# Performance work log

Measured on AMD Instinct MI355X. Metric: run time of the kernel, lower is better.

The kernel has to match this reference:

```python
import jax, jax.numpy as jnp
import numpy as np

MUL_VAL = 4.0

def _fake_quant(v, qmin, qmax):
    # per-tensor float scale from abs-max (brevitas Int8*PerTensorFloat style)
    s = jnp.max(jnp.abs(v)) / 127.0
    q = jnp.clip(jnp.round(v / s), qmin, qmax) * s
    return q

def setup_inputs() -> dict:
    key = jax.random.key(0)
    k1, k2, k3 = jax.random.split(key, 3)
    N, IN, OUT = 8192, 4096, 4096
    x = jax.random.normal(k1, (N, IN), dtype=jnp.float32)
    W = jax.random.normal(k2, (OUT, IN), dtype=jnp.float32) * 0.02
    b = jax.random.normal(k3, (OUT,), dtype=jnp.float32) * 0.01
    return {"x": x, "W": W, "b": b}

def reference(x, W, b):
    # Int8ActPerTensorFloat: signed 8-bit, non-narrow range [-128, 127]
    qx = _fake_quant(x, -128.0, 127.0)
    # Int8WeightPerTensorFloat: signed 8-bit, narrow range [-127, 127]
    qw = _fake_quant(W, -127.0, 127.0)
    y = jnp.einsum('ni,oi->no', qx, qw) + b
    return MUL_VAL * y
```

## Files before the change

### kernel.cpp

```cpp
#include <hip/hip_runtime.h>

typedef int int4v __attribute__((ext_vector_type(4)));

#define BM 128
#define BN 128
#define BK 64

__device__ __forceinline__ void async_copy16(const void* g, void* l) {
  __builtin_amdgcn_global_load_lds((const __attribute__((address_space(1))) void*)g,
                                   (__attribute__((address_space(3))) void*)l, 16, 0, 0);
}

__global__ __launch_bounds__(256) void absmax2_kernel(
    const float* __restrict__ x, size_t n4x,
    const float* __restrict__ w, size_t n4w,
    unsigned* __restrict__ out, int xb) {
  const float4* src;
  size_t n4;
  unsigned* dst;
  int bid, nb;
  if ((int)blockIdx.x < xb) {
    src = (const float4*)x; n4 = n4x; dst = out; bid = blockIdx.x; nb = xb;
  } else {
    src = (const float4*)w; n4 = n4w; dst = out + 1; bid = blockIdx.x - xb; nb = gridDim.x - xb;
  }
  size_t i = (size_t)bid * blockDim.x + threadIdx.x;
  size_t stride = (size_t)nb * blockDim.x;
  float m = 0.0f;
  for (; i < n4; i += stride) {
    float4 v = src[i];
    m = fmaxf(m, fmaxf(fmaxf(fabsf(v.x), fabsf(v.y)), fmaxf(fabsf(v.z), fabsf(v.w))));
  }
#pragma unroll
  for (int off = 32; off > 0; off >>= 1)
    m = fmaxf(m, __shfl_down(m, off, 64));
  __shared__ float red[4];
  int wave = threadIdx.x >> 6, lane = threadIdx.x & 63;
  if (lane == 0) red[wave] = m;
  __syncthreads();
  if (threadIdx.x == 0) {
    m = fmaxf(fmaxf(red[0], red[1]), fmaxf(red[2], red[3]));
    atomicMax(dst, __float_as_uint(m));
  }
}

__global__ __launch_bounds__(256) void quant2_kernel(
    const float* __restrict__ x, char* __restrict__ qx, size_t nx,
    const float* __restrict__ w, char* __restrict__ qw, size_t nw,
    const unsigned* __restrict__ amax, int xb) {
  const float* src;
  char* dst;
  size_t n;
  float r, lo;
  int bid, nb;
  if ((int)blockIdx.x < xb) {
    src = x; dst = qx; n = nx; r = 127.0f / __uint_as_float(amax[0]);
    lo = -128.0f; bid = blockIdx.x; nb = xb;
  } else {
    src = w; dst = qw; n = nw; r = 127.0f / __uint_as_float(amax[1]);
    lo = -127.0f; bid = blockIdx.x - xb; nb = gridDim.x - xb;
  }
  size_t i = ((size_t)bid * blockDim.x + threadIdx.x) * 8;
  size_t stride = (size_t)nb * blockDim.x * 8;
  for (; i < n; i += stride) {
    float4 v0 = *(const float4*)(src + i);
    float4 v1 = *(const float4*)(src + i + 4);
    float f[8] = {v0.x, v0.y, v0.z, v0.w, v1.x, v1.y, v1.z, v1.w};
    unsigned w0 = 0, w1 = 0;
#pragma unroll
    for (int j = 0; j < 4; ++j) {
      int q0 = (int)fminf(fmaxf(rintf(f[j] * r), lo), 127.0f);
      int q1 = (int)fminf(fmaxf(rintf(f[4 + j] * r), lo), 127.0f);
      w0 |= (unsigned)(q0 & 0xff) << (8 * j);
      w1 |= (unsigned)(q1 & 0xff) << (8 * j);
    }
    uint2 u; u.x = w0; u.y = w1;
    *(uint2*)(dst + i) = u;
  }
}

__global__ __launch_bounds__(256) void gemm_i8_kernel(
    const char* __restrict__ qx, const char* __restrict__ qw,
    const float* __restrict__ bias, const unsigned* __restrict__ amax,
    float* __restrict__ out, int M, int N, int K) {
  __shared__ __align__(16) char As[BM * BK];
  __shared__ __align__(16) char Bs[BN * BK];
  int tid = threadIdx.x;
  int wave = tid >> 6, lane = tid & 63;
  int wm = (wave >> 1) * 64, wn = (wave & 1) * 64;

  int tilesM = M / BM, tilesN = N / BN;
  int T = tilesM * tilesN;
  int p = blockIdx.x;
  int tile;
  if ((T & 7) == 0) tile = (p & 7) * (T >> 3) + (p >> 3);
  else tile = p;
  int bm = (tile % tilesM) * BM;
  int bn = (tile / tilesM) * BN;

  int lrow = lane >> 2;
  int lcol = (lane & 3) * 16;
  const char* gA = qx + ((size_t)bm + lrow) * K + lcol;
  const char* gB = qw + ((size_t)bn + lrow) * K + lcol;
  int c0 = wave * 2;

  int4v acc[4][4] = {};

  int r = lane & 15;
  int kb = (lane >> 4) * 16;

  for (int kt = 0; kt < K; kt += BK) {
#pragma unroll
    for (int c = 0; c < 2; ++c) {
      int cc = c0 + c;
      async_copy16(gA + (size_t)(cc * 16) * K + kt, As + cc * 1024);
      async_copy16(gB + (size_t)(cc * 16) * K + kt, Bs + cc * 1024);
    }
    __syncthreads();
    int4v a[4], b[4];
#pragma unroll
    for (int i = 0; i < 4; ++i)
      a[i] = *(const int4v*)(As + (size_t)(wm + i * 16 + r) * BK + kb);
#pragma unroll
    for (int j = 0; j < 4; ++j)
      b[j] = *(const int4v*)(Bs + (size_t)(wn + j * 16 + r) * BK + kb);
#pragma unroll
    for (int i = 0; i < 4; ++i)
#pragma unroll
      for (int j = 0; j < 4; ++j)
        acc[i][j] = __builtin_amdgcn_mfma_i32_16x16x64_i8(a[i], b[j], acc[i][j], 0, 0, 0);
    __syncthreads();
  }

  float sx = __uint_as_float(amax[0]) / 127.0f;
  float sw = __uint_as_float(amax[1]) / 127.0f;
  float scale = 4.0f * sx * sw;
  int col = lane & 15;
  int rq = (lane >> 4) * 4;
#pragma unroll
  for (int j = 0; j < 4; ++j) {
    int gn = bn + wn + j * 16 + col;
    float b4 = 4.0f * bias[gn];
#pragma unroll
    for (int i = 0; i < 4; ++i) {
      size_t base = (size_t)(bm + wm + i * 16 + rq) * N + gn;
#pragma unroll
      for (int rr = 0; rr < 4; ++rr)
        __builtin_nontemporal_store(scale * (float)acc[i][j][rr] + b4,
                                    out + base + (size_t)rr * N);
    }
  }
}

extern "C" void kernel_launch(void* const* d_in, const int* in_sizes, int n_in,
                              void* d_out, int out_size, void* d_ws, size_t ws_size,
                              hipStream_t stream) {
  const float* x = (const float*)d_in[0];
  const float* W = (const float*)d_in[1];
  const float* b = (const float*)d_in[2];
  float* out = (float*)d_out;

  int Nv = in_sizes[2];
  int K = in_sizes[1] / Nv;
  int M = in_sizes[0] / K;

  size_t nx = (size_t)M * K, nw = (size_t)Nv * K;
  unsigned* amax = (unsigned*)d_ws;
  char* qx = (char*)d_ws + 256;
  char* qw = qx + nx;

  hipMemsetAsync(d_ws, 0, 8, stream);
  absmax2_kernel<<<1536, 256, 0, stream>>>(x, nx / 4, W, nw / 4, amax, 1024);
  quant2_kernel<<<3072, 256, 0, stream>>>(x, qx, nx, W, qw, nw, amax, 2048);
  gemm_i8_kernel<<<(M / BM) * (Nv / BN), 256, 0, stream>>>(qx, qw, b, amax, out, M, Nv, K);
}
```

Baseline: 488.0 us.

## Rewrite int8 GEMM with 256x256 tiles, double-buffered LDS and phased MFMA pipeline

The int8 GEMM moves from 128x128x64 single-buffered tiles to 256x256x128 tiles with 8 waves, double-buffered LDS, XOR-swizzled LDS layout, and an 8-phase schedule that interleaves async global-to-LDS staging with MFMA bursts under setprio and explicit vmcnt waits. The aim is to hide global load latency behind compute, raise arithmetic intensity per tile and avoid LDS bank conflicts. It uses 128 KB of LDS per block and many accumulator registers, which limits occupancy, and it needs K to be a multiple of 256 for the unrolled loop.

```diff
diff --git a/kernel.cpp b/kernel.cpp
--- a/kernel.cpp
+++ b/kernel.cpp
@@ -2,9 +2,9 @@
 
 typedef int int4v __attribute__((ext_vector_type(4)));
 
-#define BM 128
-#define BN 128
-#define BK 64
+#define BM 256
+#define BN 256
+#define BKB 128
 
 __device__ __forceinline__ void async_copy16(const void* g, void* l) {
   __builtin_amdgcn_global_load_lds((const __attribute__((address_space(1))) void*)g,
@@ -79,15 +79,80 @@
   }
 }
 
-__global__ __launch_bounds__(256) void gemm_i8_kernel(
+
+#define STAGE_A(buf_, t_, rowb_) do {                                          \
+    int r0_ = (rowb_) + wave * 8;                                              \
+    async_copy16(gA + (size_t)r0_ * K + (size_t)(t_) * BKB,                    \
+                 &As[buf_][r0_ * BKB]);                                        \
+    async_copy16(gA + (size_t)(r0_ + 64) * K + (size_t)(t_) * BKB,             \
+                 &As[buf_][(r0_ + 64) * BKB]);                                 \
+  } while (0)
+
+#define STAGE_B(buf_, t_, rowb_) do {                                          \
+    int r0_ = (rowb_) + wave * 8;                                              \
+    async_copy16(gB + (size_t)r0_ * K + (size_t)(t_) * BKB,                    \
+                 &Bs[buf_][r0_ * BKB]);                                        \
+    async_copy16(gB + (size_t)(r0_ + 64) * K + (size_t)(t_) * BKB,             \
+                 &Bs[buf_][(r0_ + 64) * BKB]);                                 \
+  } while (0)
+
+#define VM4 asm volatile("s_waitcnt vmcnt(4)" ::: "memory")
+#define VM0 asm volatile("s_waitcnt vmcnt(0)" ::: "memory")
+#define VMN ((void)0)
+#define NOSTG ((void)0)
+
+#define MFMA_I8 __builtin_amdgcn_mfma_i32_16x16x64_i8
+
+#define PHASE(bb_, mh_, nh_, STG, VMW) do {                                    \
+    asm volatile("" ::: "memory");                                             \
+    const char* Ab_ = &As[bb_][((mh_)*128 + wr * 64 + r16) * BKB];             \
+    const char* Bb_ = &Bs[bb_][((nh_)*128 + wc * 32 + r16) * BKB];             \
+    int4v a00_ = *(const int4v*)(Ab_ + 0 * 16 * BKB + slot0);                  \
+    int4v a01_ = *(const int4v*)(Ab_ + 0 * 16 * BKB + slot1);                  \
+    int4v a10_ = *(const int4v*)(Ab_ + 1 * 16 * BKB + slot0);                  \
+    int4v a11_ = *(const int4v*)(Ab_ + 1 * 16 * BKB + slot1);                  \
+    int4v a20_ = *(const int4v*)(Ab_ + 2 * 16 * BKB + slot0);                  \
+    int4v a21_ = *(const int4v*)(Ab_ + 2 * 16 * BKB + slot1);                  \
+    int4v a30_ = *(const int4v*)(Ab_ + 3 * 16 * BKB + slot0);                  \
+    int4v a31_ = *(const int4v*)(Ab_ + 3 * 16 * BKB + slot1);                  \
+    int4v b00_ = *(const int4v*)(Bb_ + 0 * 16 * BKB + slot0);                  \
+    int4v b01_ = *(const int4v*)(Bb_ + 0 * 16 * BKB + slot1);                  \
+    int4v b10_ = *(const int4v*)(Bb_ + 1 * 16 * BKB + slot0);                  \
+    int4v b11_ = *(const int4v*)(Bb_ + 1 * 16 * BKB + slot1);                  \
+    STG;                                                                       \
+    __builtin_amdgcn_s_barrier();                                              \
+    __builtin_amdgcn_s_setprio(1);                                             \
+    acc[mh_][nh_][0][0] = MFMA_I8(a00_, b00_, acc[mh_][nh_][0][0], 0, 0, 0);   \
+    acc[mh_][nh_][0][0] = MFMA_I8(a01_, b01_, acc[mh_][nh_][0][0], 0, 0, 0);   \
+    acc[mh_][nh_][0][1] = MFMA_I8(a00_, b10_, acc[mh_][nh_][0][1], 0, 0, 0);   \
+    acc[mh_][nh_][0][1] = MFMA_I8(a01_, b11_, acc[mh_][nh_][0][1], 0, 0, 0);   \
+    acc[mh_][nh_][1][0] = MFMA_I8(a10_, b00_, acc[mh_][nh_][1][0], 0, 0, 0);   \
+    acc[mh_][nh_][1][0] = MFMA_I8(a11_, b01_, acc[mh_][nh_][1][0], 0, 0, 0);   \
+    acc[mh_][nh_][1][1] = MFMA_I8(a10_, b10_, acc[mh_][nh_][1][1], 0, 0, 0);   \
+    acc[mh_][nh_][1][1] = MFMA_I8(a11_, b11_, acc[mh_][nh_][1][1], 0, 0, 0);   \
+    acc[mh_][nh_][2][0] = MFMA_I8(a20_, b00_, acc[mh_][nh_][2][0], 0, 0, 0);   \
+    acc[mh_][nh_][2][0] = MFMA_I8(a21_, b01_, acc[mh_][nh_][2][0], 0, 0, 0);   \
+    acc[mh_][nh_][2][1] = MFMA_I8(a20_, b10_, acc[mh_][nh_][2][1], 0, 0, 0);   \
+    acc[mh_][nh_][2][1] = MFMA_I8(a21_, b11_, acc[mh_][nh_][2][1], 0, 0, 0);   \
+    acc[mh_][nh_][3][0] = MFMA_I8(a30_, b00_, acc[mh_][nh_][3][0], 0, 0, 0);   \
+    acc[mh_][nh_][3][0] = MFMA_I8(a31_, b01_, acc[mh_][nh_][3][0], 0, 0, 0);   \
+    acc[mh_][nh_][3][1] = MFMA_I8(a30_, b10_, acc[mh_][nh_][3][1], 0, 0, 0);   \
+    acc[mh_][nh_][3][1] = MFMA_I8(a31_, b11_, acc[mh_][nh_][3][1], 0, 0, 0);   \
+    __builtin_amdgcn_s_setprio(0);                                             \
+    VMW;                                                                       \
+    asm volatile("" ::: "memory");                                             \
+    __builtin_amdgcn_s_barrier();                                              \
+  } while (0)
+
+__global__ __launch_bounds__(512, 2) void gemm_i8_kernel(
     const char* __restrict__ qx, const char* __restrict__ qw,
     const float* __restrict__ bias, const unsigned* __restrict__ amax,
     float* __restrict__ out, int M, int N, int K) {
-  __shared__ __align__(16) char As[BM * BK];
-  __shared__ __align__(16) char Bs[BN * BK];
-  int tid = threadIdx.x;
-  int wave = tid >> 6, lane = tid & 63;
-  int wm = (wave >> 1) * 64, wn = (wave & 1) * 64;
+  __shared__ __align__(16) char As[2][BM * BKB];
+  __shared__ __align__(16) char Bs[2][BN * BKB];
+  const int tid = threadIdx.x;
+  const int wave = tid >> 6, lane = tid & 63;
+  const int wr = wave >> 2, wc = wave & 3;
 
   int tilesM = M / BM, tilesN = N / BN;
   int T = tilesM * tilesN;
@@ -98,58 +163,71 @@
   int bm = (tile % tilesM) * BM;
   int bn = (tile / tilesM) * BN;
 
-  int lrow = lane >> 2;
-  int lcol = (lane & 3) * 16;
-  const char* gA = qx + ((size_t)bm + lrow) * K + lcol;
-  const char* gB = qw + ((size_t)bn + lrow) * K + lcol;
-  int c0 = wave * 2;
-
-  int4v acc[4][4] = {};
-
-  int r = lane & 15;
-  int kb = (lane >> 4) * 16;
-
-  for (int kt = 0; kt < K; kt += BK) {
-#pragma unroll
-    for (int c = 0; c < 2; ++c) {
-      int cc = c0 + c;
-      async_copy16(gA + (size_t)(cc * 16) * K + kt, As + cc * 1024);
-      async_copy16(gB + (size_t)(cc * 16) * K + kt, Bs + cc * 1024);
-    }
-    __syncthreads();
-    int4v a[4], b[4];
-#pragma unroll
-    for (int i = 0; i < 4; ++i)
-      a[i] = *(const int4v*)(As + (size_t)(wm + i * 16 + r) * BK + kb);
-#pragma unroll
-    for (int j = 0; j < 4; ++j)
-      b[j] = *(const int4v*)(Bs + (size_t)(wn + j * 16 + r) * BK + kb);
-#pragma unroll
-    for (int i = 0; i < 4; ++i)
-#pragma unroll
-      for (int j = 0; j < 4; ++j)
-        acc[i][j] = __builtin_amdgcn_mfma_i32_16x16x64_i8(a[i], b[j], acc[i][j], 0, 0, 0);
-    __syncthreads();
-  }
-
-  float sx = __uint_as_float(amax[0]) / 127.0f;
-  float sw = __uint_as_float(amax[1]) / 127.0f;
-  float scale = 4.0f * sx * sw;
-  int col = lane & 15;
-  int rq = (lane >> 4) * 4;
-#pragma unroll
-  for (int j = 0; j < 4; ++j) {
-    int gn = bn + wn + j * 16 + col;
-    float b4 = 4.0f * bias[gn];
-#pragma unroll
-    for (int i = 0; i < 4; ++i) {
-      size_t base = (size_t)(bm + wm + i * 16 + rq) * N + gn;
-#pragma unroll
-      for (int rr = 0; rr < 4; ++rr)
-        __builtin_nontemporal_store(scale * (float)acc[i][j][rr] + b4,
-                                    out + base + (size_t)rr * N);
-    }
-  }
+  const int grow = lane >> 3;
+  const int gcol = ((lane & 7) ^ grow) * 16;
+  const char* gA = qx + (size_t)(bm + grow) * K + gcol;
+  const char* gB = qw + (size_t)(bn + grow) * K + gcol;
+
+  const int r16 = lane & 15, hi = lane >> 4;
+  const int slot0 = ((0 + hi) ^ (lane & 7)) * 16;
+  const int slot1 = ((4 + hi) ^ (lane & 7)) * 16;
+
+  const int NT = K >> 7;
+
+  int4v acc[2][2][4][2] = {};
+
+  STAGE_A(0, 0, 0);
+  STAGE_B(0, 0, 0);
+  STAGE_A(0, 0, 128);
+  STAGE_B(0, 0, 128);
+  STAGE_A(1, 1, 0);
+  STAGE_B(1, 1, 0);
+  VM4;
+  __builtin_amdgcn_s_barrier();
+
+  int t = 0;
+  for (; t + 3 < NT; t += 2) {
+    PHASE(0, 0, 0, STAGE_A(1, t + 1, 128), VMN);
+    PHASE(0, 0, 1, STAGE_B(1, t + 1, 128), VMN);
+    PHASE(0, 1, 0, STAGE_A(0, t + 2, 0), VMN);
+    PHASE(0, 1, 1, STAGE_B(0, t + 2, 0), VM4);
+    PHASE(1, 0, 0, STAGE_A(0, t + 2, 128), VMN);
+    PHASE(1, 0, 1, STAGE_B(0, t + 2, 128), VMN);
+    PHASE(1, 1, 0, STAGE_A(1, t + 3, 0), VMN);
+    PHASE(1, 1, 1, STAGE_B(1, t + 3, 0), VM4);
+  }
+  PHASE(0, 0, 0, STAGE_A(1, NT - 1, 128), VMN);
+  PHASE(0, 0, 1, STAGE_B(1, NT - 1, 128), VMN);
+  PHASE(0, 1, 0, NOSTG, VMN);
+  PHASE(0, 1, 1, NOSTG, VM0);
+  PHASE(1, 0, 0, NOSTG, VMN);
+  PHASE(1, 0, 1, NOSTG, VMN);
+  PHASE(1, 1, 0, NOSTG, VMN);
+  PHASE(1, 1, 1, NOSTG, VMN);
+
+  float fx = __uint_as_float(amax[0]) * (1.0f / 127.0f);
+  float fw = __uint_as_float(amax[1]) * (1.0f / 127.0f);
+  float scale = 4.0f * fx * fw;
+  int col16 = lane & 15;
+  int rq = (lane >> 4) << 2;
+#pragma unroll
+  for (int mh = 0; mh < 2; ++mh)
+#pragma unroll
+    for (int nh = 0; nh < 2; ++nh)
+#pragma unroll
+      for (int n = 0; n < 2; ++n) {
+        int gn = bn + nh * 128 + wc * 32 + n * 16 + col16;
+        float b4 = 4.0f * bias[gn];
+#pragma unroll
+        for (int m = 0; m < 4; ++m) {
+          size_t base = (size_t)(bm + mh * 128 + wr * 64 + m * 16 + rq) * N + gn;
+#pragma unroll
+          for (int rr = 0; rr < 4; ++rr)
+            __builtin_nontemporal_store(
+                scale * (float)acc[mh][nh][m][n][rr] + b4,
+                out + base + (size_t)rr * N);
+        }
+      }
 }
 
 extern "C" void kernel_launch(void* const* d_in, const int* in_sizes, int n_in,
@@ -172,5 +250,5 @@
   hipMemsetAsync(d_ws, 0, 8, stream);
   absmax2_kernel<<<1536, 256, 0, stream>>>(x, nx / 4, W, nw / 4, amax, 1024);
   quant2_kernel<<<3072, 256, 0, stream>>>(x, qx, nx, W, qw, nw, amax, 2048);
-  gemm_i8_kernel<<<(M / BM) * (Nv / BN), 256, 0, stream>>>(qx, qw, b, amax, out, M, Nv, K);
-}
+  gemm_i8_kernel<<<(M / BM) * (Nv / BN), 512, 0, stream>>>(qx, qw, b, amax, out, M, Nv, K);
+}
```

Result: faster. 459.1 us (-5.9%).

## Rewrite int8 GEMM with 256x256 tiles, double-buffered LDS, swizzle, 32x32 MFMA

Applied to the files above, without the earlier changes.

Rebuilds the int8 GEMM around 256x256x128 block tiles with 512 threads. It double-buffers LDS so global-to-LDS async copies overlap MFMA compute, XOR-swizzles the LDS layout to avoid bank conflicts, and switches to 32x32x32 i8 MFMAs with raised wave priority. This targets the original kernel's low data reuse and the stall caused by its synchronous per-tile load-then-compute loop. In exchange it uses much more LDS (128 KB per block) and more registers, which limits occupancy, and the loop assumes K is a multiple of 256.

```diff
diff --git a/kernel.cpp b/kernel.cpp
--- a/kernel.cpp
+++ b/kernel.cpp
@@ -1,10 +1,11 @@
 #include <hip/hip_runtime.h>
 
 typedef int int4v __attribute__((ext_vector_type(4)));
-
-#define BM 128
-#define BN 128
-#define BK 64
+typedef int int16v __attribute__((ext_vector_type(16)));
+
+#define BM 256
+#define BN 256
+#define BKB 128
 
 __device__ __forceinline__ void async_copy16(const void* g, void* l) {
   __builtin_amdgcn_global_load_lds((const __attribute__((address_space(1))) void*)g,
@@ -79,15 +80,62 @@
   }
 }
 
-__global__ __launch_bounds__(256) void gemm_i8_kernel(
+
+#define STAGE_ALL(buf_, t_) do {                                               \
+    const char* ga_ = gA + (size_t)(t_) * BKB;                                 \
+    const char* gb_ = gB + (size_t)(t_) * BKB;                                 \
+    int r0_ = wave * 8;                                                        \
+    async_copy16(ga_ + (size_t)(r0_      ) * K, &As[buf_][(r0_      ) * BKB]); \
+    async_copy16(ga_ + (size_t)(r0_ +  64) * K, &As[buf_][(r0_ +  64) * BKB]); \
+    async_copy16(ga_ + (size_t)(r0_ + 128) * K, &As[buf_][(r0_ + 128) * BKB]); \
+    async_copy16(ga_ + (size_t)(r0_ + 192) * K, &As[buf_][(r0_ + 192) * BKB]); \
+    async_copy16(gb_ + (size_t)(r0_      ) * K, &Bs[buf_][(r0_      ) * BKB]); \
+    async_copy16(gb_ + (size_t)(r0_ +  64) * K, &Bs[buf_][(r0_ +  64) * BKB]); \
+    async_copy16(gb_ + (size_t)(r0_ + 128) * K, &Bs[buf_][(r0_ + 128) * BKB]); \
+    async_copy16(gb_ + (size_t)(r0_ + 192) * K, &Bs[buf_][(r0_ + 192) * BKB]); \
+  } while (0)
+
+#define VM0 asm volatile("s_waitcnt vmcnt(0)" ::: "memory")
+#define BAR do { asm volatile("" ::: "memory");                                \
+                 __builtin_amdgcn_s_barrier();                                 \
+                 asm volatile("" ::: "memory"); } while (0)
+
+#define MFMA32 __builtin_amdgcn_mfma_i32_32x32x32_i8
+
+#define KSTEP(so_) do {                                                        \
+    int4v a0_ = *(const int4v*)(Ab_ + 0 * 32 * BKB + (so_));                   \
+    int4v a1_ = *(const int4v*)(Ab_ + 1 * 32 * BKB + (so_));                   \
+    int4v a2_ = *(const int4v*)(Ab_ + 2 * 32 * BKB + (so_));                   \
+    int4v a3_ = *(const int4v*)(Ab_ + 3 * 32 * BKB + (so_));                   \
+    int4v b0_ = *(const int4v*)(Bb_ + 0 * 32 * BKB + (so_));                   \
+    int4v b1_ = *(const int4v*)(Bb_ + 1 * 32 * BKB + (so_));                   \
+    __builtin_amdgcn_s_setprio(1);                                             \
+    acc[0][0] = MFMA32(a0_, b0_, acc[0][0], 0, 0, 0);                          \
+    acc[0][1] = MFMA32(a0_, b1_, acc[0][1], 0, 0, 0);                          \
+    acc[1][0] = MFMA32(a1_, b0_, acc[1][0], 0, 0, 0);                          \
+    acc[1][1] = MFMA32(a1_, b1_, acc[1][1], 0, 0, 0);                          \
+    acc[2][0] = MFMA32(a2_, b0_, acc[2][0], 0, 0, 0);                          \
+    acc[2][1] = MFMA32(a2_, b1_, acc[2][1], 0, 0, 0);                          \
+    acc[3][0] = MFMA32(a3_, b0_, acc[3][0], 0, 0, 0);                          \
+    acc[3][1] = MFMA32(a3_, b1_, acc[3][1], 0, 0, 0);                          \
+    __builtin_amdgcn_s_setprio(0);                                             \
+  } while (0)
+
+#define COMPUTE(bb_) do {                                                      \
+    const char* Ab_ = &As[bb_][(wr * 128 + r32) * BKB];                        \
+    const char* Bb_ = &Bs[bb_][(wc * 64 + r32) * BKB];                         \
+    KSTEP(so0); KSTEP(so1); KSTEP(so2); KSTEP(so3);                            \
+  } while (0)
+
+__global__ __launch_bounds__(512, 2) void gemm_i8_kernel(
     const char* __restrict__ qx, const char* __restrict__ qw,
     const float* __restrict__ bias, const unsigned* __restrict__ amax,
     float* __restrict__ out, int M, int N, int K) {
-  __shared__ __align__(16) char As[BM * BK];
-  __shared__ __align__(16) char Bs[BN * BK];
-  int tid = threadIdx.x;
-  int wave = tid >> 6, lane = tid & 63;
-  int wm = (wave >> 1) * 64, wn = (wave & 1) * 64;
+  __shared__ __align__(16) char As[2][BM * BKB];
+  __shared__ __align__(16) char Bs[2][BN * BKB];
+  const int tid = threadIdx.x;
+  const int wave = tid >> 6, lane = tid & 63;
+  const int wr = wave >> 2, wc = wave & 3;
 
   int tilesM = M / BM, tilesN = N / BN;
   int T = tilesM * tilesN;
@@ -98,56 +146,58 @@
   int bm = (tile % tilesM) * BM;
   int bn = (tile / tilesM) * BN;
 
-  int lrow = lane >> 2;
-  int lcol = (lane & 3) * 16;
-  const char* gA = qx + ((size_t)bm + lrow) * K + lcol;
-  const char* gB = qw + ((size_t)bn + lrow) * K + lcol;
-  int c0 = wave * 2;
-
-  int4v acc[4][4] = {};
-
-  int r = lane & 15;
-  int kb = (lane >> 4) * 16;
-
-  for (int kt = 0; kt < K; kt += BK) {
-#pragma unroll
-    for (int c = 0; c < 2; ++c) {
-      int cc = c0 + c;
-      async_copy16(gA + (size_t)(cc * 16) * K + kt, As + cc * 1024);
-      async_copy16(gB + (size_t)(cc * 16) * K + kt, Bs + cc * 1024);
-    }
-    __syncthreads();
-    int4v a[4], b[4];
-#pragma unroll
-    for (int i = 0; i < 4; ++i)
-      a[i] = *(const int4v*)(As + (size_t)(wm + i * 16 + r) * BK + kb);
-#pragma unroll
-    for (int j = 0; j < 4; ++j)
-      b[j] = *(const int4v*)(Bs + (size_t)(wn + j * 16 + r) * BK + kb);
-#pragma unroll
-    for (int i = 0; i < 4; ++i)
-#pragma unroll
-      for (int j = 0; j < 4; ++j)
-        acc[i][j] = __builtin_amdgcn_mfma_i32_16x16x64_i8(a[i], b[j], acc[i][j], 0, 0, 0);
-    __syncthreads();
-  }
-
-  float sx = __uint_as_float(amax[0]) / 127.0f;
-  float sw = __uint_as_float(amax[1]) / 127.0f;
-  float scale = 4.0f * sx * sw;
-  int col = lane & 15;
-  int rq = (lane >> 4) * 4;
-#pragma unroll
-  for (int j = 0; j < 4; ++j) {
-    int gn = bn + wn + j * 16 + col;
+  const int grow = lane >> 3;
+  const int gcol = ((lane & 7) ^ grow) * 16;
+  const char* gA = qx + (size_t)(bm + grow) * K + gcol;
+  const char* gB = qw + (size_t)(bn + grow) * K + gcol;
+
+  const int r32 = lane & 31, hi = lane >> 5, l7 = lane & 7;
+  const int so0 = ((0 + hi) ^ l7) * 16;
+  const int so1 = ((2 + hi) ^ l7) * 16;
+  const int so2 = ((4 + hi) ^ l7) * 16;
+  const int so3 = ((6 + hi) ^ l7) * 16;
+
+  const int NT = K >> 7;
+
+  int16v acc[4][2] = {};
+
+  STAGE_ALL(0, 0);
+  VM0;
+  BAR;
+
+  int t = 0;
+  for (; t < NT - 2; t += 2) {
+    STAGE_ALL(1, t + 1);
+    COMPUTE(0);
+    VM0; BAR;
+    STAGE_ALL(0, t + 2);
+    COMPUTE(1);
+    VM0; BAR;
+  }
+  STAGE_ALL(1, NT - 1);
+  COMPUTE(0);
+  VM0; BAR;
+  COMPUTE(1);
+
+  float fx = __uint_as_float(amax[0]) * (1.0f / 127.0f);
+  float fw = __uint_as_float(amax[1]) * (1.0f / 127.0f);
+  float scale = 4.0f * fx * fw;
+  int col = lane & 31;
+  int rbh = 4 * hi;
+#pragma unroll
+  for (int n = 0; n < 2; ++n) {
+    int gn = bn + wc * 64 + n * 32 + col;
     float b4 = 4.0f * bias[gn];
 #pragma unroll
-    for (int i = 0; i < 4; ++i) {
-      size_t base = (size_t)(bm + wm + i * 16 + rq) * N + gn;
-#pragma unroll
-      for (int rr = 0; rr < 4; ++rr)
-        __builtin_nontemporal_store(scale * (float)acc[i][j][rr] + b4,
-                                    out + base + (size_t)rr * N);
+    for (int m = 0; m < 4; ++m) {
+      size_t rowb = (size_t)(bm + wr * 128 + m * 32 + rbh);
+#pragma unroll
+      for (int g = 0; g < 4; ++g)
+#pragma unroll
+        for (int rr = 0; rr < 4; ++rr)
+          __builtin_nontemporal_store(
+              scale * (float)acc[m][n][g * 4 + rr] + b4,
+              out + (rowb + g * 8 + rr) * N + gn);
     }
   }
 }
@@ -172,5 +222,5 @@
   hipMemsetAsync(d_ws, 0, 8, stream);
   absmax2_kernel<<<1536, 256, 0, stream>>>(x, nx / 4, W, nw / 4, amax, 1024);
   quant2_kernel<<<3072, 256, 0, stream>>>(x, qx, nx, W, qw, nw, amax, 2048);
-  gemm_i8_kernel<<<(M / BM) * (Nv / BN), 256, 0, stream>>>(qx, qw, b, amax, out, M, Nv, K);
-}
+  gemm_i8_kernel<<<(M / BM) * (Nv / BN), 512, 0, stream>>>(qx, qw, b, amax, out, M, Nv, K);
+}
```

New measurement: 442.8 us. -9.3%, faster.
